# Optimization experiments

Measured on AMD Instinct MI355X. Metric: run time of the kernel, lower is better.

## Reference

```python
import jax, jax.numpy as jnp
import numpy as np

EMB = 256; HID = 256
N_TEXT = 80000; N_NON = 20000; N = N_TEXT + N_NON
E = 300000; R = 2000; L = 8; MV = 17; MD = 64
ROUNDS = 2; REV_ROUNDS = 2


def _scatter_mean(x, src, dst, n):
    # PyG MessagePassing(aggr='mean'): out[i] = mean of x[src] over edges with dst==i (0 if none)
    s = jax.ops.segment_sum(x[src], dst, num_segments=n)
    cnt = jax.ops.segment_sum(jnp.ones(src.shape, x.dtype), dst, num_segments=n)
    return s / jnp.maximum(cnt, 1.0)[:, None]


def setup_inputs() -> dict:
    key = jax.random.key(0)
    ks = jax.random.split(key, 24)
    inp = {}
    inp['h_id_tensor'] = jax.random.randint(ks[0], (E,), 0, N)
    inp['r_id_tensor'] = jax.random.randint(ks[1], (E,), 0, R)
    inp['t_id_tensor'] = jax.random.randint(ks[2], (E,), 0, N)
    inp['q_emb'] = jax.random.normal(ks[3], (1, EMB), jnp.float32)
    inp['entity_embs'] = jax.random.normal(ks[4], (N_TEXT, EMB), jnp.float32)
    inp['num_non_text_entities'] = N_NON
    inp['relation_embs'] = jax.random.normal(ks[5], (R, EMB), jnp.float32)
    topic = (jax.random.uniform(ks[6], (N,)) < 0.001).astype(jnp.float32)
    inp['topic_entity_one_hot'] = jnp.stack([topic, 1.0 - topic], axis=1)  # [N, 2]
    inp['triple_motif_token_ids'] = jax.random.randint(ks[7], (E, L), 0, MV)
    inp['triple_motif_token_wts'] = jax.random.uniform(ks[8], (E, L), jnp.float32)
    s = 0.02
    inp['non_text_emb'] = jax.random.normal(ks[9], (1, EMB), jnp.float32) * s
    inp['motif_emb'] = jax.random.normal(ks[10], (MV, MD), jnp.float32) * s
    POS_D = 2 + 2 * (ROUNDS + REV_ROUNDS)  # 10
    inp['W_nb'] = jax.random.normal(ks[11], (2 * EMB, HID), jnp.float32) * s
    inp['b_nb'] = jnp.zeros((HID,), jnp.float32)
    inp['W_pos'] = jax.random.normal(ks[12], (2 * POS_D, HID), jnp.float32) * s
    inp['b_pos'] = jnp.zeros((HID,), jnp.float32)
    inp['W_str'] = jax.random.normal(ks[13], (EMB + MD, HID), jnp.float32) * s
    inp['b_str'] = jnp.zeros((HID,), jnp.float32)
    inp['W_gate'] = jax.random.normal(ks[14], (EMB, 3), jnp.float32) * s
    inp['b_gate'] = jnp.zeros((3,), jnp.float32)
    inp['W1'] = jax.random.normal(ks[15], (EMB + HID, HID), jnp.float32) * s
    inp['b1'] = jnp.zeros((HID,), jnp.float32)
    inp['W2'] = jax.random.normal(ks[16], (HID, 1), jnp.float32) * s
    inp['b2'] = jnp.zeros((1,), jnp.float32)
    return inp


def reference(h_id_tensor, r_id_tensor, t_id_tensor, q_emb, entity_embs,
              num_non_text_entities, relation_embs, topic_entity_one_hot,
              triple_motif_token_ids, triple_motif_token_wts,
              non_text_emb, motif_emb,
              W_nb, b_nb, W_pos, b_pos, W_str, b_str, W_gate, b_gate,
              W1, b1, W2, b2):
    n = entity_embs.shape[0] + num_non_text_entities
    emb = entity_embs.shape[1]
    # node embeddings: text entities + shared non-text embedding row
    h_e = jnp.concatenate([
        entity_embs,
        jnp.broadcast_to(non_text_emb[0], (num_non_text_entities, emb)),
    ], axis=0)
    # DDE: multi-round scatter-mean propagation on forward and reversed edges
    dde_list = []
    h = topic_entity_one_hot
    for _ in range(ROUNDS):
        h = _scatter_mean(h, h_id_tensor, t_id_tensor, n)
        dde_list.append(h)
    h = topic_entity_one_hot
    for _ in range(REV_ROUNDS):
        h = _scatter_mean(h, t_id_tensor, h_id_tensor, n)
        dde_list.append(h)
    h_r = relation_embs[r_id_tensor]  # [E, emb]
    # motif embedding (padding_idx=0 -> zero row)
    me = motif_emb.at[0].set(0.0)
    triple_motif = jnp.einsum('eld,el->ed', me[triple_motif_token_ids], triple_motif_token_wts)
    # channel heads
    h_h = h_e[h_id_tensor]
    h_t = h_e[t_id_tensor]
    h_neigh = jax.nn.relu(jnp.concatenate([h_h, h_t], axis=1) @ W_nb + b_nb)
    pos = jnp.concatenate([topic_entity_one_hot] + dde_list, axis=1)  # [N, 10]
    h_posn = jax.nn.relu(jnp.concatenate([pos[h_id_tensor], pos[t_id_tensor]], axis=1) @ W_pos + b_pos)
    h_struct = jax.nn.relu(jnp.concatenate([h_r, triple_motif], axis=1) @ W_str + b_str)
    # softmax gate over 3 channels from the query embedding
    gate = jax.nn.softmax((q_emb @ W_gate + b_gate)[0], axis=0)  # [3]
    h_fused = gate[0] * h_neigh + gate[1] * h_posn + gate[2] * h_struct
    pred_in = jnp.concatenate([jnp.broadcast_to(q_emb, (h_r.shape[0], emb)), h_fused], axis=1)
    pred = jax.nn.relu(pred_in @ W1 + b1) @ W2 + b2  # [E, 1]
    return pred
```

## Files before the change

### kernel.cpp

```cpp
#include <hip/hip_runtime.h>

#define EMB 256
typedef unsigned short u16;
typedef __attribute__((ext_vector_type(8))) short short8v;
typedef __attribute__((ext_vector_type(4))) short short4v;
typedef __attribute__((ext_vector_type(4))) float f32x4;

__device__ inline u16 f2bf(float x){
  union{float f; unsigned u;} c; c.f = x;
  unsigned r = c.u + 0x7FFFu + ((c.u>>16)&1u);
  return (u16)(r>>16);
}
__device__ inline float bf2f(u16 h){
  union{unsigned u; float f;} c; c.u = ((unsigned)h) << 16; return c.f;
}

__global__ void k_scatter1(const int* __restrict__ h_id, const int* __restrict__ t_id,
                           const float* __restrict__ topic,
                           float* __restrict__ cnt_f, float* __restrict__ cnt_r,
                           float* __restrict__ accf, float* __restrict__ accr, int E) {
  int e = blockIdx.x * 256 + threadIdx.x;
  if (e >= E) return;
  int h = h_id[e], t = t_id[e];
  atomicAdd(&cnt_f[t], 1.0f);
  atomicAdd(&cnt_r[h], 1.0f);
  float a0 = topic[2*h+0], a1 = topic[2*h+1];
  if (a0 != 0.f) atomicAdd(&accf[2*t+0], a0);
  if (a1 != 0.f) atomicAdd(&accf[2*t+1], a1);
  float c0 = topic[2*t+0], c1 = topic[2*t+1];
  if (c0 != 0.f) atomicAdd(&accr[2*h+0], c0);
  if (c1 != 0.f) atomicAdd(&accr[2*h+1], c1);
}

__global__ void k_div1_gate(const float* __restrict__ topic,
                            const float* __restrict__ cnt_f, const float* __restrict__ cnt_r,
                            const float* __restrict__ accf, const float* __restrict__ accr,
                            float* __restrict__ pos, int N,
                            const float* __restrict__ q, const float* __restrict__ Wg,
                            const float* __restrict__ bg, const float* __restrict__ W1,
                            const float* __restrict__ b1, float* __restrict__ gateq) {
  int t = threadIdx.x;
  if (blockIdx.x == 0) {
    __shared__ float qs[256];
    __shared__ float z[3];
    qs[t] = q[t];
    __syncthreads();
    if (t < 3) {
      float s = bg[t];
      for (int k = 0; k < 256; ++k) s += qs[k] * Wg[k*3 + t];
      z[t] = s;
    }
    __syncthreads();
    if (t == 0) {
      float m = fmaxf(z[0], fmaxf(z[1], z[2]));
      float e0 = expf(z[0]-m), e1 = expf(z[1]-m), e2 = expf(z[2]-m);
      float s = e0 + e1 + e2;
      gateq[0] = e0/s; gateq[1] = e1/s; gateq[2] = e2/s; gateq[3] = 0.f;
    }
    float a = b1[t];
    for (int k = 0; k < 256; ++k) a += qs[k] * W1[k*256 + t];
    gateq[4 + t] = a;
    return;
  }
  int n = (blockIdx.x - 1) * 256 + t;
  if (n >= N) return;
  float cf = fmaxf(cnt_f[n], 1.0f), cr = fmaxf(cnt_r[n], 1.0f);
  pos[10*n+0] = topic[2*n+0];
  pos[10*n+1] = topic[2*n+1];
  pos[10*n+2] = accf[2*n+0] / cf;
  pos[10*n+3] = accf[2*n+1] / cf;
  pos[10*n+6] = accr[2*n+0] / cr;
  pos[10*n+7] = accr[2*n+1] / cr;
}

__global__ void k_scatter2(const int* __restrict__ h_id, const int* __restrict__ t_id,
                           const float* __restrict__ pos,
                           float* __restrict__ accf, float* __restrict__ accr, int E) {
  int e = blockIdx.x * 256 + threadIdx.x;
  if (e >= E) return;
  int h = h_id[e], t = t_id[e];
  float a0 = pos[10*h+2], a1 = pos[10*h+3];
  if (a0 != 0.f) atomicAdd(&accf[2*t+0], a0);
  if (a1 != 0.f) atomicAdd(&accf[2*t+1], a1);
  float c0 = pos[10*t+6], c1 = pos[10*t+7];
  if (c0 != 0.f) atomicAdd(&accr[2*h+0], c0);
  if (c1 != 0.f) atomicAdd(&accr[2*h+1], c1);
}

__global__ void k_div2(const float* __restrict__ cnt_f, const float* __restrict__ cnt_r,
                       const float* __restrict__ accf, const float* __restrict__ accr,
                       float* __restrict__ pos, int N) {
  int n = blockIdx.x * 256 + threadIdx.x;
  if (n >= N) return;
  float cf = fmaxf(cnt_f[n], 1.0f), cr = fmaxf(cnt_r[n], 1.0f);
  pos[10*n+4] = accf[2*n+0] / cf;
  pos[10*n+5] = accf[2*n+1] / cf;
  pos[10*n+8] = accr[2*n+0] / cr;
  pos[10*n+9] = accr[2*n+1] / cr;
}

__global__ void k_wtrans(const float* __restrict__ Wpos, const float* __restrict__ Wstr,
                         const float* __restrict__ W1, const float* __restrict__ Wnb,
                         const float* __restrict__ bpos, const float* __restrict__ motif,
                         const float* __restrict__ gateq,
                         u16* __restrict__ WB, u16* __restrict__ WN) {
  int gid = blockIdx.x * 256 + threadIdx.x;
  if (gid < 10*1024) {
    int lane = gid & 63, ft = (gid >> 6) & 15, kt = gid >> 10;
    int n  = ft*16 + (lane & 15);
    int k0 = (lane >> 4) * 8;
    short8v v;
    if (kt == 0) {
      float g1 = gateq[1];
      #pragma unroll
      for (int j = 0; j < 8; ++j) {
        int k = k0 + j;
        float x = (k < 20) ? g1 * Wpos[(size_t)k*256 + n]
                : (k == 20) ? g1 * bpos[n] : 0.f;
        v[j] = (short)f2bf(x);
      }
    } else if (kt == 1) {
      float g2 = gateq[2];
      #pragma unroll
      for (int j = 0; j < 8; ++j) {
        int m = k0 + j;
        float x = 0.f;
        if (m >= 1 && m < 17) {
          float a = 0.f;
          for (int k = 0; k < 64; ++k)
            a = fmaf(motif[(size_t)m*64 + k], Wstr[(size_t)(256+k)*256 + n], a);
          x = g2 * a;
        }
        v[j] = (short)f2bf(x);
      }
    } else {
      int kb = (kt - 2) * 32;
      #pragma unroll
      for (int j = 0; j < 8; ++j)
        v[j] = (short)f2bf(W1[(size_t)(256 + kb + k0 + j)*256 + n]);
    }
    *(short8v*)(WB + (size_t)gid * 8) = v;
  } else {
    int g = gid - 10240;
    if (g >= 8*32*64) return;
    int lane = g & 63, nt = (g >> 6) & 31, kc = g >> 11;
    int col = nt*16 + (lane & 15);
    int k0  = kc*32 + (lane >> 4) * 8;
    short8v v;
    #pragma unroll
    for (int j = 0; j < 8; ++j) {
      int k = k0 + j;
      float x = (col < 256) ? Wnb[(size_t)k*256 + col] : Wnb[(size_t)(256+k)*256 + (col-256)];
      v[j] = (short)f2bf(x);
    }
    *(short8v*)(WN + (size_t)g * 8) = v;
  }
}

__global__ __launch_bounds__(512) void k_node_S(const float* __restrict__ ent,
                                                const float* __restrict__ ntx,
                                                const u16* __restrict__ WN,
                                                u16* __restrict__ TA, u16* __restrict__ TB,
                                                int NT, int nNodeBlk,
                                                const float* __restrict__ rel,
                                                const float* __restrict__ Wstr,
                                                const float* __restrict__ b_nb,
                                                const float* __restrict__ b_str,
                                                const float* __restrict__ gateq,
                                                float* __restrict__ S) {
  const int t = threadIdx.x;
  if ((int)blockIdx.x >= nNodeBlk) {
    __shared__ float rs[2][256];
    int half = t >> 8, tc = t & 255;
    int r = (blockIdx.x - nNodeBlk) * 2 + half;
    rs[half][tc] = rel[(size_t)r*256 + tc];
    __syncthreads();
    float a = 0.f;
    for (int k = 0; k < 256; ++k) a = fmaf(rs[half][k], Wstr[(size_t)k*256 + tc], a);
    S[(size_t)r*256 + tc] = gateq[2] * (a + b_str[tc]);
    return;
  }
  __shared__ __align__(16) u16 AF[4*64*8];
  __shared__ __align__(16) u16 TT[64*512];
  const int wv = t >> 6, l = t & 63;
  const int lr = l & 15, lg = l >> 4;
  const int nb0 = blockIdx.x * 64;
  const float g0 = gateq[0];

  const int mt = t >> 7, half = (t >> 6) & 1, l2 = t & 63;
  int snode = nb0 + mt*16 + (l2 & 15);
  const float* srow = (snode < NT) ? (ent + (size_t)snode * EMB) : ntx;

  f32x4 acc[4][4];
  #pragma unroll
  for (int m = 0; m < 4; ++m)
    #pragma unroll
    for (int n = 0; n < 4; ++n) acc[m][n] = (f32x4){0.f,0.f,0.f,0.f};

  for (int kc = 0; kc < 8; ++kc) {
    {
      int k = kc*32 + (l2 >> 4)*8 + half*4;
      float4 a4 = *(const float4*)(srow + k);
      short4v v;
      v[0]=(short)f2bf(a4.x); v[1]=(short)f2bf(a4.y);
      v[2]=(short)f2bf(a4.z); v[3]=(short)f2bf(a4.w);
      *(short4v*)&AF[((mt*64 + l2)*8 + half*4)] = v;
    }
    __syncthreads();
    short8v bn[4], af[4];
    #pragma unroll
    for (int n = 0; n < 4; ++n)
      bn[n] = *(const short8v*)&WN[((size_t)(kc*32 + wv*4 + n)*64 + l)*8];
    #pragma unroll
    for (int m = 0; m < 4; ++m)
      af[m] = *(const short8v*)&AF[(m*64 + l)*8];
    #pragma unroll
    for (int m = 0; m < 4; ++m)
      #pragma unroll
      for (int n = 0; n < 4; ++n)
        acc[m][n] = __builtin_amdgcn_mfma_f32_16x16x32_bf16(af[m], bn[n], acc[m][n], 0, 0, 0);
    __syncthreads();
  }
  #pragma unroll
  for (int m = 0; m < 4; ++m)
    #pragma unroll
    for (int n = 0; n < 4; ++n) {
      int col = wv*64 + n*16 + lr;
      float bias = (col < 256) ? b_nb[col] : 0.f;
      #pragma unroll
      for (int r2 = 0; r2 < 4; ++r2)
        TT[(m*16 + lg*4 + r2)*512 + col] = f2bf(g0 * (acc[m][n][r2] + bias));
    }
  __syncthreads();
  #pragma unroll
  for (int p = 0; p < 8; ++p) {
    int idx = p*512 + t;
    int nrow = idx >> 6, col = (idx & 63)*8;
    int node = nb0 + nrow;
    if (node <= NT) {
      uint4 v = *(const uint4*)&TT[nrow*512 + col];
      u16* dst = (col < 256) ? (TA + (size_t)node*256 + col)
                             : (TB + (size_t)node*256 + (col-256));
      *(uint4*)dst = v;
    }
  }
}

__global__ __launch_bounds__(256, 4)
void k_main(
    const int* __restrict__ h_id, const int* __restrict__ r_id, const int* __restrict__ t_id,
    const int* __restrict__ mids, const float* __restrict__ mwts,
    const float* __restrict__ W2, const float* __restrict__ b2,
    const float* __restrict__ pos, const float* __restrict__ gateq,
    const u16* __restrict__ WB, const float* __restrict__ S,
    const u16* __restrict__ TA, const u16* __restrict__ TB,
    float* __restrict__ out, int E, int NT)
{
  __shared__ __align__(16) u16 SH[20480];
  u16* FT2 = SH;
  u16* XB  = SH + 16384;
  u16* XB2 = SH + 18432;
  float* woacc = (float*)(SH + 16384);

  const int t  = threadIdx.x;
  const int wv = t >> 6, l = t & 63;
  const int Mw = wv >> 1, Nw = wv & 1;
  const int lr = l & 15, lg = l >> 4;
  const int be = blockIdx.x * 64;

  int eo = be + wv*16 + lr; if (eo >= E) eo = E - 1;
  const int hid = h_id[eo], tid = t_id[eo];

  {
    const int hc = (hid < NT) ? hid : NT;
    const u16* paw = TA + (size_t)hc*256 + lg*8;
    #pragma unroll
    for (int kc = 0; kc < 8; ++kc)
      __builtin_amdgcn_global_load_lds(
        (const __attribute__((address_space(1))) unsigned int*)(paw + kc*32),
        (__attribute__((address_space(3))) unsigned int*)&FT2[kc*2048 + wv*512],
        16, 0, 0);
  }

  {
    float vals[8];
    #pragma unroll
    for (int jp = 0; jp < 4; ++jp) {
      int k2 = lg*8 + jp*2;
      float2 f2;
      if (k2 < 10)       f2 = *(const float2*)&pos[(size_t)hid*10 + k2];
      else if (k2 < 20)  f2 = *(const float2*)&pos[(size_t)tid*10 + (k2 - 10)];
      else if (k2 == 20) f2 = make_float2(1.f, 0.f);
      else               f2 = make_float2(0.f, 0.f);
      vals[jp*2] = f2.x; vals[jp*2+1] = f2.y;
    }
    short8v v;
    #pragma unroll
    for (int j = 0; j < 8; ++j) v[j] = (short)f2bf(vals[j]);
    *(short8v*)&XB[(wv*64 + l)*8] = v;
  }

  {
    int4   mi0 = *(const int4*)  (mids + (size_t)eo*8);
    int4   mi1 = *(const int4*)  (mids + (size_t)eo*8 + 4);
    float4 mw0 = *(const float4*)(mwts + (size_t)eo*8);
    float4 mw1 = *(const float4*)(mwts + (size_t)eo*8 + 4);
    int   idv[8] = {mi0.x,mi0.y,mi0.z,mi0.w,mi1.x,mi1.y,mi1.z,mi1.w};
    float wtv[8] = {mw0.x,mw0.y,mw0.z,mw0.w,mw1.x,mw1.y,mw1.z,mw1.w};
    float s[8] = {0,0,0,0,0,0,0,0};
    #pragma unroll
    for (int j = 0; j < 8; ++j)
      #pragma unroll
      for (int i = 0; i < 8; ++i)
        s[i] += (idv[j] == lg*8 + i) ? wtv[j] : 0.f;
    short8v v;
    #pragma unroll
    for (int i = 0; i < 8; ++i) v[i] = (short)f2bf(s[i]);
    *(short8v*)&XB2[(wv*64 + l)*8] = v;
  }

  {
    const int tc2 = (tid < NT) ? tid : NT;
    const u16* pbw = TB + (size_t)tc2*256 + lg*8;
    short8v tb0 = *(const short8v*)(pbw);
    short8v tb1 = *(const short8v*)(pbw + 32);
    asm volatile("s_waitcnt vmcnt(0)" ::: "memory");
    __builtin_amdgcn_sched_barrier(0);
    #pragma unroll
    for (int kk = 0; kk < 8; kk += 2) {
      short8v nba = tb0, nbb = tb1;
      if (kk < 6) {
        tb0 = *(const short8v*)(pbw + (kk+2)*32);
        tb1 = *(const short8v*)(pbw + (kk+3)*32);
      }
      #pragma unroll
      for (int c2 = 0; c2 < 2; ++c2) {
        short8v nb = c2 ? nbb : nba;
        u16* slot = &FT2[((kk+c2)*4 + wv)*512 + l*8];
        short8v o = *(const short8v*)slot;
        short8v w;
        #pragma unroll
        for (int j = 0; j < 8; ++j)
          w[j] = (short)f2bf(fmaxf(bf2f((u16)o[j]) + bf2f((u16)nb[j]), 0.f));
        *(short8v*)slot = w;
      }
    }
  }

  f32x4 acc[8][2];
  auto zacc = [&]() {
    #pragma unroll
    for (int m = 0; m < 8; ++m)
      #pragma unroll
      for (int n = 0; n < 2; ++n) acc[m][n] = (f32x4){0.f,0.f,0.f,0.f};
  };
  auto mfma_chunk = [&](const u16* wc, const u16* xb) {
    short8v bfr[2];
    #pragma unroll
    for (int n = 0; n < 2; ++n)
      bfr[n] = *(const short8v*)&xb[((Nw*2 + n)*64 + l)*8];
    #pragma unroll
    for (int mh = 0; mh < 8; mh += 4) {
      short8v af[4];
      #pragma unroll
      for (int mm = 0; mm < 4; ++mm)
        af[mm] = *(const short8v*)&wc[((Mw*8 + mh + mm)*64 + l)*8];
      #pragma unroll
      for (int mm = 0; mm < 4; ++mm)
        #pragma unroll
        for (int n = 0; n < 2; ++n)
          acc[mh+mm][n] = __builtin_amdgcn_mfma_f32_16x16x32_bf16(af[mm], bfr[n], acc[mh+mm][n], 0, 0, 0);
    }
  };

  zacc();
  __syncthreads();

  mfma_chunk(WB, XB);
  {
    #pragma unroll
    for (int m = 0; m < 8; ++m) {
      int kc  = Mw*4 + ((m*4 + lg) >> 3);
      int lg2 = (m*2 + (lg >> 1)) & 3;
      #pragma unroll
      for (int n = 0; n < 2; ++n) {
        int nt = Nw*2 + n;
        int idx = ((kc*4 + nt)*64 + lg2*16 + lr)*8 + (lg & 1)*4;
        short4v o = *(const short4v*)&FT2[idx];
        short4v w;
        w[0] = (short)f2bf(bf2f((u16)o[0]) + fmaxf(acc[m][n][0], 0.f));
        w[1] = (short)f2bf(bf2f((u16)o[1]) + fmaxf(acc[m][n][1], 0.f));
        w[2] = (short)f2bf(bf2f((u16)o[2]) + fmaxf(acc[m][n][2], 0.f));
        w[3] = (short)f2bf(bf2f((u16)o[3]) + fmaxf(acc[m][n][3], 0.f));
        *(short4v*)&FT2[idx] = w;
      }
    }
  }
  zacc();

  mfma_chunk(WB + 8192, XB2);
  {
    int r0 = be + (Nw*2 + 0)*16 + lr; if (r0 >= E) r0 = E - 1;
    int r1 = be + (Nw*2 + 1)*16 + lr; if (r1 >= E) r1 = E - 1;
    int rr[2] = { r_id[r0], r_id[r1] };
    #pragma unroll
    for (int m = 0; m < 8; ++m) {
      int f0 = Mw*128 + m*16 + lg*4;
      int kc  = Mw*4 + ((m*4 + lg) >> 3);
      int lg2 = (m*2 + (lg >> 1)) & 3;
      #pragma unroll
      for (int n = 0; n < 2; ++n) {
        int nt = Nw*2 + n;
        float4 sv = *(const float4*)&S[(size_t)rr[n]*256 + f0];
        int idx = ((kc*4 + nt)*64 + lg2*16 + lr)*8 + (lg & 1)*4;
        short4v o = *(const short4v*)&FT2[idx];
        short4v w;
        w[0] = (short)f2bf(bf2f((u16)o[0]) + fmaxf(acc[m][n][0] + sv.x, 0.f));
        w[1] = (short)f2bf(bf2f((u16)o[1]) + fmaxf(acc[m][n][1] + sv.y, 0.f));
        w[2] = (short)f2bf(bf2f((u16)o[2]) + fmaxf(acc[m][n][2] + sv.z, 0.f));
        w[3] = (short)f2bf(bf2f((u16)o[3]) + fmaxf(acc[m][n][3] + sv.w, 0.f));
        *(short4v*)&FT2[idx] = w;
      }
    }
  }

  #pragma unroll
  for (int m = 0; m < 8; ++m) {
    int f0 = Mw*128 + m*16 + lg*4;
    float4 q4 = *(const float4*)&gateq[4 + f0];
    f32x4 qv = { q4.x, q4.y, q4.z, q4.w };
    acc[m][0] = qv; acc[m][1] = qv;
  }
  __syncthreads();
  for (int c2 = 0; c2 < 8; ++c2) {
    const u16* wc = WB + (size_t)(2 + c2) * 8192;
    short8v bfr[2];
    #pragma unroll
    for (int n = 0; n < 2; ++n)
      bfr[n] = *(const short8v*)&FT2[((c2*4 + Nw*2 + n)*64 + l)*8];
    #pragma unroll
    for (int mh = 0; mh < 8; mh += 4) {
      short8v af[4];
      #pragma unroll
      for (int mm = 0; mm < 4; ++mm)
        af[mm] = *(const short8v*)&wc[((Mw*8 + mh + mm)*64 + l)*8];
      #pragma unroll
      for (int mm = 0; mm < 4; ++mm)
        #pragma unroll
        for (int n = 0; n < 2; ++n)
          acc[mh+mm][n] = __builtin_amdgcn_mfma_f32_16x16x32_bf16(af[mm], bfr[n], acc[mh+mm][n], 0, 0, 0);
    }
  }

  {
    #pragma unroll
    for (int n = 0; n < 2; ++n) {
      float p = 0.f;
      #pragma unroll
      for (int m = 0; m < 8; ++m) {
        int f0 = Mw*128 + m*16 + lg*4;
        float4 w4 = *(const float4*)&W2[f0];
        p = fmaf(fmaxf(acc[m][n][0], 0.f), w4.x, p);
        p = fmaf(fmaxf(acc[m][n][1], 0.f), w4.y, p);
        p = fmaf(fmaxf(acc[m][n][2], 0.f), w4.z, p);
        p = fmaf(fmaxf(acc[m][n][3], 0.f), w4.w, p);
      }
      p += __shfl_xor(p, 16);
      p += __shfl_xor(p, 32);
      if (lg == 0) woacc[Mw*64 + Nw*32 + n*16 + lr] = p;
    }
  }
  __syncthreads();
  if (t < 64) {
    int e = be + t;
    if (e < E)
      out[e] = woacc[t] + woacc[64 + t] + b2[0];
  }
}

extern "C" void kernel_launch(void* const* d_in, const int* in_sizes, int n_in,
                              void* d_out, int out_size, void* d_ws, size_t ws_size,
                              hipStream_t stream) {
  const int*   h_id  = (const int*)  d_in[0];
  const int*   r_id  = (const int*)  d_in[1];
  const int*   t_id  = (const int*)  d_in[2];
  const float* q     = (const float*)d_in[3];
  const float* ent   = (const float*)d_in[4];
  const float* rel   = (const float*)d_in[6];
  const float* topic = (const float*)d_in[7];
  const int*   mids  = (const int*)  d_in[8];
  const float* mwts  = (const float*)d_in[9];
  const float* ntx   = (const float*)d_in[10];
  const float* motif = (const float*)d_in[11];
  const float* W_nb  = (const float*)d_in[12];
  const float* b_nb  = (const float*)d_in[13];
  const float* W_pos = (const float*)d_in[14];
  const float* b_pos = (const float*)d_in[15];
  const float* W_str = (const float*)d_in[16];
  const float* b_str = (const float*)d_in[17];
  const float* W_g   = (const float*)d_in[18];
  const float* b_g   = (const float*)d_in[19];
  const float* W1    = (const float*)d_in[20];
  const float* b1    = (const float*)d_in[21];
  const float* W2    = (const float*)d_in[22];
  const float* b2    = (const float*)d_in[23];
  float* out = (float*)d_out;

  const int E  = in_sizes[0];
  const int NT = in_sizes[4] / EMB;
  const int N  = in_sizes[7] / 2;

  float* ws    = (float*)d_ws;
  float* cnt_f = ws;
  float* cnt_r = ws + (size_t)N;
  float* a1f   = ws + (size_t)2*N;
  float* a1r   = ws + (size_t)4*N;
  float* a2f   = ws + (size_t)6*N;
  float* a2r   = ws + (size_t)8*N;
  float* pos   = ws + (size_t)10*N;
  float* gateq = ws + (size_t)20*N;
  u16*   WB    = (u16*)(ws + (size_t)20*N + 512);
  u16*   WN    = WB + (size_t)10*8192;
  float* S     = (float*)(WN + 131072);
  u16*   TA    = (u16*)(S + (size_t)2000*256);
  u16*   TB    = TA + (size_t)(NT+1)*256;

  hipMemsetAsync(d_ws, 0, (size_t)10 * N * sizeof(float), stream);

  int gE = (E + 255) / 256, gN = (N + 255) / 256;
  int nNodeBlk = (NT + 64) / 64;
  k_scatter1 <<<gE, 256, 0, stream>>>(h_id, t_id, topic, cnt_f, cnt_r, a1f, a1r, E);
  k_div1_gate<<<gN + 1, 256, 0, stream>>>(topic, cnt_f, cnt_r, a1f, a1r, pos, N,
                                          q, W_g, b_g, W1, b1, gateq);
  k_scatter2 <<<gE, 256, 0, stream>>>(h_id, t_id, pos, a2f, a2r, E);
  k_div2     <<<gN, 256, 0, stream>>>(cnt_f, cnt_r, a2f, a2r, pos, N);
  k_wtrans   <<<104, 256, 0, stream>>>(W_pos, W_str, W1, W_nb, b_pos, motif, gateq,
                                       WB, WN);
  k_node_S   <<<nNodeBlk + 1000, 512, 0, stream>>>(ent, ntx, WN, TA, TB, NT, nNodeBlk,
                                                   rel, W_str, b_nb, b_str, gateq, S);

  int gM = (E + 63) / 64;
  k_main<<<gM, 256, 0, stream>>>(h_id, r_id, t_id, mids, mwts,
                                 W2, b2, pos, gateq, WB, S, TA, TB, out, E, NT);
}
```

Baseline: 333.5 us.

## Fold second divide into node kernel, use packed bf16 conversion, prefetch node rows

Removes the separate k_div2 launch by adding extra blocks to k_node_S that compute the second-round mean division. Replaces the scalar float-to-bf16 rounding code with the v_cvt_pk_bf16_f32 packed conversion instruction in several places in k_main and k_node_S. Also software-prefetches the next entity row chunk in the node GEMM loop. These target launch overhead and ALU cost in conversion-heavy epilogues. The hardware conversion's rounding may differ slightly from the hand-written routine, for example on NaN inputs.

Result: faster. 321.2 us (-3.7%).

```diff
diff --git a/kernel.cpp b/kernel.cpp
--- a/kernel.cpp
+++ b/kernel.cpp
@@ -13,6 +13,16 @@
 }
 __device__ inline float bf2f(u16 h){
   union{unsigned u; float f;} c; c.u = ((unsigned)h) << 16; return c.f;
+}
+__device__ inline unsigned pk2(float a, float b){
+  unsigned r;
+  asm("v_cvt_pk_bf16_f32 %0, %1, %2" : "=v"(r) : "v"(a), "v"(b));
+  return r;
+}
+__device__ inline void unpk(unsigned d, float& lo, float& hi){
+  union{unsigned u; float f;} a, b;
+  a.u = d << 16; b.u = d & 0xffff0000u;
+  lo = a.f; hi = b.f;
 }
 
 __global__ void k_scatter1(const int* __restrict__ h_id, const int* __restrict__ t_id,
@@ -87,18 +97,6 @@
   if (c1 != 0.f) atomicAdd(&accr[2*h+1], c1);
 }
 
-__global__ void k_div2(const float* __restrict__ cnt_f, const float* __restrict__ cnt_r,
-                       const float* __restrict__ accf, const float* __restrict__ accr,
-                       float* __restrict__ pos, int N) {
-  int n = blockIdx.x * 256 + threadIdx.x;
-  if (n >= N) return;
-  float cf = fmaxf(cnt_f[n], 1.0f), cr = fmaxf(cnt_r[n], 1.0f);
-  pos[10*n+4] = accf[2*n+0] / cf;
-  pos[10*n+5] = accf[2*n+1] / cf;
-  pos[10*n+8] = accr[2*n+0] / cr;
-  pos[10*n+9] = accr[2*n+1] / cr;
-}
-
 __global__ void k_wtrans(const float* __restrict__ Wpos, const float* __restrict__ Wstr,
                          const float* __restrict__ W1, const float* __restrict__ Wnb,
                          const float* __restrict__ bpos, const float* __restrict__ motif,
@@ -167,8 +165,23 @@
                                                 const float* __restrict__ b_nb,
                                                 const float* __restrict__ b_str,
                                                 const float* __restrict__ gateq,
+                                                const float* __restrict__ cnt_f,
+                                                const float* __restrict__ cnt_r,
+                                                const float* __restrict__ a2f,
+                                                const float* __restrict__ a2r,
+                                                float* __restrict__ posw, int N,
                                                 float* __restrict__ S) {
   const int t = threadIdx.x;
+  if ((int)blockIdx.x >= nNodeBlk + 1000) {
+    int n = ((int)blockIdx.x - nNodeBlk - 1000) * 512 + t;
+    if (n >= N) return;
+    float cf = fmaxf(cnt_f[n], 1.0f), cr = fmaxf(cnt_r[n], 1.0f);
+    posw[10*n+4] = a2f[2*n+0] / cf;
+    posw[10*n+5] = a2f[2*n+1] / cf;
+    posw[10*n+8] = a2r[2*n+0] / cr;
+    posw[10*n+9] = a2r[2*n+1] / cr;
+    return;
+  }
   if ((int)blockIdx.x >= nNodeBlk) {
     __shared__ float rs[2][256];
     int half = t >> 8, tc = t & 255;
@@ -190,6 +203,7 @@
   const int mt = t >> 7, half = (t >> 6) & 1, l2 = t & 63;
   int snode = nb0 + mt*16 + (l2 & 15);
   const float* srow = (snode < NT) ? (ent + (size_t)snode * EMB) : ntx;
+  const int off = (l2 >> 4)*8 + half*4;
 
   f32x4 acc[4][4];
   #pragma unroll
@@ -197,14 +211,13 @@
     #pragma unroll
     for (int n = 0; n < 4; ++n) acc[m][n] = (f32x4){0.f,0.f,0.f,0.f};
 
+  float4 nxt = *(const float4*)(srow + off);
   for (int kc = 0; kc < 8; ++kc) {
+    float4 cur = nxt;
+    if (kc < 7) nxt = *(const float4*)(srow + (kc+1)*32 + off);
     {
-      int k = kc*32 + (l2 >> 4)*8 + half*4;
-      float4 a4 = *(const float4*)(srow + k);
-      short4v v;
-      v[0]=(short)f2bf(a4.x); v[1]=(short)f2bf(a4.y);
-      v[2]=(short)f2bf(a4.z); v[3]=(short)f2bf(a4.w);
-      *(short4v*)&AF[((mt*64 + l2)*8 + half*4)] = v;
+      unsigned d0 = pk2(cur.x, cur.y), d1 = pk2(cur.z, cur.w);
+      *(uint2*)&AF[((mt*64 + l2)*8 + half*4)] = make_uint2(d0, d1);
     }
     __syncthreads();
     short8v bn[4], af[4];
@@ -294,10 +307,9 @@
       else               f2 = make_float2(0.f, 0.f);
       vals[jp*2] = f2.x; vals[jp*2+1] = f2.y;
     }
-    short8v v;
-    #pragma unroll
-    for (int j = 0; j < 8; ++j) v[j] = (short)f2bf(vals[j]);
-    *(short8v*)&XB[(wv*64 + l)*8] = v;
+    uint4 v = { pk2(vals[0],vals[1]), pk2(vals[2],vals[3]),
+                pk2(vals[4],vals[5]), pk2(vals[6],vals[7]) };
+    *(uint4*)&XB[(wv*64 + l)*8] = v;
   }
 
   {
@@ -313,36 +325,35 @@
       #pragma unroll
       for (int i = 0; i < 8; ++i)
         s[i] += (idv[j] == lg*8 + i) ? wtv[j] : 0.f;
-    short8v v;
-    #pragma unroll
-    for (int i = 0; i < 8; ++i) v[i] = (short)f2bf(s[i]);
-    *(short8v*)&XB2[(wv*64 + l)*8] = v;
+    uint4 v = { pk2(s[0],s[1]), pk2(s[2],s[3]), pk2(s[4],s[5]), pk2(s[6],s[7]) };
+    *(uint4*)&XB2[(wv*64 + l)*8] = v;
   }
 
   {
     const int tc2 = (tid < NT) ? tid : NT;
-    const u16* pbw = TB + (size_t)tc2*256 + lg*8;
-    short8v tb0 = *(const short8v*)(pbw);
-    short8v tb1 = *(const short8v*)(pbw + 32);
+    const uint4* pb4 = (const uint4*)(TB + (size_t)tc2*256 + lg*8);
+    uint4 tb0 = pb4[0];
+    uint4 tb1 = pb4[4];
     asm volatile("s_waitcnt vmcnt(0)" ::: "memory");
     __builtin_amdgcn_sched_barrier(0);
+    auto fuse = [](unsigned od, unsigned nd)->unsigned {
+      float ol, oh, nl, nh;
+      unpk(od, ol, oh); unpk(nd, nl, nh);
+      return pk2(fmaxf(ol + nl, 0.f), fmaxf(oh + nh, 0.f));
+    };
     #pragma unroll
     for (int kk = 0; kk < 8; kk += 2) {
-      short8v nba = tb0, nbb = tb1;
-      if (kk < 6) {
-        tb0 = *(const short8v*)(pbw + (kk+2)*32);
-        tb1 = *(const short8v*)(pbw + (kk+3)*32);
-      }
+      uint4 nba = tb0, nbb = tb1;
+      if (kk < 6) { tb0 = pb4[(kk+2)*4]; tb1 = pb4[(kk+3)*4]; }
       #pragma unroll
       for (int c2 = 0; c2 < 2; ++c2) {
-        short8v nb = c2 ? nbb : nba;
-        u16* slot = &FT2[((kk+c2)*4 + wv)*512 + l*8];
-        short8v o = *(const short8v*)slot;
-        short8v w;
-        #pragma unroll
-        for (int j = 0; j < 8; ++j)
-          w[j] = (short)f2bf(fmaxf(bf2f((u16)o[j]) + bf2f((u16)nb[j]), 0.f));
-        *(short8v*)slot = w;
+        uint4 nb = c2 ? nbb : nba;
+        uint4* slot = (uint4*)&FT2[((kk+c2)*4 + wv)*512 + l*8];
+        uint4 o = *slot;
+        uint4 w;
+        w.x = fuse(o.x, nb.x); w.y = fuse(o.y, nb.y);
+        w.z = fuse(o.z, nb.z); w.w = fuse(o.w, nb.w);
+        *slot = w;
       }
     }
   }
@@ -386,13 +397,13 @@
       for (int n = 0; n < 2; ++n) {
         int nt = Nw*2 + n;
         int idx = ((kc*4 + nt)*64 + lg2*16 + lr)*8 + (lg & 1)*4;
-        short4v o = *(const short4v*)&FT2[idx];
-        short4v w;
-        w[0] = (short)f2bf(bf2f((u16)o[0]) + fmaxf(acc[m][n][0], 0.f));
-        w[1] = (short)f2bf(bf2f((u16)o[1]) + fmaxf(acc[m][n][1], 0.f));
-        w[2] = (short)f2bf(bf2f((u16)o[2]) + fmaxf(acc[m][n][2], 0.f));
-        w[3] = (short)f2bf(bf2f((u16)o[3]) + fmaxf(acc[m][n][3], 0.f));
-        *(short4v*)&FT2[idx] = w;
+        uint2* sp2 = (uint2*)&FT2[idx];
+        uint2 o = *sp2;
+        float ol, oh, pl, ph;
+        unpk(o.x, ol, oh); unpk(o.y, pl, ph);
+        o.x = pk2(ol + fmaxf(acc[m][n][0], 0.f), oh + fmaxf(acc[m][n][1], 0.f));
+        o.y = pk2(pl + fmaxf(acc[m][n][2], 0.f), ph + fmaxf(acc[m][n][3], 0.f));
+        *sp2 = o;
       }
     }
   }
@@ -413,13 +424,15 @@
         int nt = Nw*2 + n;
         float4 sv = *(const float4*)&S[(size_t)rr[n]*256 + f0];
         int idx = ((kc*4 + nt)*64 + lg2*16 + lr)*8 + (lg & 1)*4;
-        short4v o = *(const short4v*)&FT2[idx];
-        short4v w;
-        w[0] = (short)f2bf(bf2f((u16)o[0]) + fmaxf(acc[m][n][0] + sv.x, 0.f));
-        w[1] = (short)f2bf(bf2f((u16)o[1]) + fmaxf(acc[m][n][1] + sv.y, 0.f));
-        w[2] = (short)f2bf(bf2f((u16)o[2]) + fmaxf(acc[m][n][2] + sv.z, 0.f));
-        w[3] = (short)f2bf(bf2f((u16)o[3]) + fmaxf(acc[m][n][3] + sv.w, 0.f));
-        *(short4v*)&FT2[idx] = w;
+        uint2* sp2 = (uint2*)&FT2[idx];
+        uint2 o = *sp2;
+        float ol, oh, pl, ph;
+        unpk(o.x, ol, oh); unpk(o.y, pl, ph);
+        o.x = pk2(ol + fmaxf(acc[m][n][0] + sv.x, 0.f),
+                  oh + fmaxf(acc[m][n][1] + sv.y, 0.f));
+        o.y = pk2(pl + fmaxf(acc[m][n][2] + sv.z, 0.f),
+                  ph + fmaxf(acc[m][n][3] + sv.w, 0.f));
+        *sp2 = o;
       }
     }
   }
@@ -529,15 +542,16 @@
 
   int gE = (E + 255) / 256, gN = (N + 255) / 256;
   int nNodeBlk = (NT + 64) / 64;
+  int gD = (N + 511) / 512;
   k_scatter1 <<<gE, 256, 0, stream>>>(h_id, t_id, topic, cnt_f, cnt_r, a1f, a1r, E);
   k_div1_gate<<<gN + 1, 256, 0, stream>>>(topic, cnt_f, cnt_r, a1f, a1r, pos, N,
                                           q, W_g, b_g, W1, b1, gateq);
   k_scatter2 <<<gE, 256, 0, stream>>>(h_id, t_id, pos, a2f, a2r, E);
-  k_div2     <<<gN, 256, 0, stream>>>(cnt_f, cnt_r, a2f, a2r, pos, N);
   k_wtrans   <<<104, 256, 0, stream>>>(W_pos, W_str, W1, W_nb, b_pos, motif, gateq,
                                        WB, WN);
-  k_node_S   <<<nNodeBlk + 1000, 512, 0, stream>>>(ent, ntx, WN, TA, TB, NT, nNodeBlk,
-                                                   rel, W_str, b_nb, b_str, gateq, S);
+  k_node_S   <<<nNodeBlk + 1000 + gD, 512, 0, stream>>>(ent, ntx, WN, TA, TB, NT, nNodeBlk,
+                                                        rel, W_str, b_nb, b_str, gateq,
+                                                        cnt_f, cnt_r, a2f, a2r, pos, N, S);
 
   int gM = (E + 63) / 64;
   k_main<<<gM, 256, 0, stream>>>(h_id, r_id, t_id, mids, mwts,
```
